# Optimization experiments

Hardware: AMD Instinct MI355X
Metric: run time of the kernel (lower is better)

## Reference

```python
import jax, jax.numpy as jnp
import numpy as np

N = 100_000      # nodes
E = 1_600_000    # edges (avg degree 16)
P = 100_000      # pos/neg sampled edges
L = 3            # GIN layers
D_IN = 128
D_H = 128
D_MLP = 512
D_PRED = D_H // 2
D_FIN = 1


def setup_inputs() -> dict:
    key = jax.random.key(0)
    ks = jax.random.split(key, 12)
    s_in = 1.0 / np.sqrt(D_IN)
    s_mlp = 1.0 / np.sqrt(D_MLP)
    s_h = 1.0 / np.sqrt(D_H)
    s_p = 1.0 / np.sqrt(D_PRED)
    return {
        "x":   jax.random.normal(ks[0], (N, D_IN), jnp.float32),
        "W1":  jax.random.normal(ks[1], (L, D_IN, D_MLP), jnp.float32) * s_in,
        "b1":  jnp.zeros((L, D_MLP), jnp.float32),
        "W2":  jax.random.normal(ks[2], (L, D_MLP, D_H), jnp.float32) * s_mlp,
        "b2":  jnp.zeros((L, D_H), jnp.float32),
        "Wp1": jax.random.normal(ks[3], (D_H, D_PRED), jnp.float32) * s_h,
        "bp1": jnp.zeros((D_PRED,), jnp.float32),
        "Wp2": jax.random.normal(ks[4], (D_PRED, D_FIN), jnp.float32) * s_p,
        "bp2": jnp.zeros((D_FIN,), jnp.float32),
        "edge_src": jax.random.randint(ks[5], (E,), 0, N),
        "edge_dst": jax.random.randint(ks[6], (E,), 0, N),
        "pos_src": jax.random.randint(ks[7], (P,), 0, N),
        "pos_dst": jax.random.randint(ks[8], (P,), 0, N),
        "neg_src": jax.random.randint(ks[9], (P,), 0, N),
        "neg_dst": jax.random.randint(ks[10], (P,), 0, N),
    }


def reference(x, W1, b1, W2, b2, Wp1, bp1, Wp2, bp2,
              edge_src, edge_dst, pos_src, pos_dst, neg_src, neg_dst):
    h = x
    for l in range(L):
        # GINConv 'sum': aggregate neighbor features src->dst, eps=0
        agg = jax.ops.segment_sum(h[edge_src], edge_dst, num_segments=N)
        z = jax.nn.relu((h + agg) @ W1[l] + b1[l])   # [N, D_MLP]
        h = z @ W2[l] + b2[l]                        # [N, D_H]
        h = jax.nn.relu(h)                           # outer ReLU in forward()

    def predict(src, dst):
        z = jax.nn.relu((h[src] * h[dst]) @ Wp1 + bp1)
        return z @ Wp2 + bp2                         # [P, D_FIN]

    h_pos = predict(pos_src, pos_dst)
    h_neg = predict(neg_src, neg_dst)
    return (h_pos, h_neg, h)
```

## Files before the change

kernel.cpp:

```cpp
#include <hip/hip_runtime.h>

typedef unsigned short ushort_t;

constexpr int NN = 100000;
constexpr int EE = 1600000;
constexpr int PP = 100000;
constexpr int DH = 128;
constexpr int DM = 512;

using frag_b16 = __attribute__((ext_vector_type(8))) short;
using frag_f32 = __attribute__((ext_vector_type(4))) float;

union FragU {
  ushort_t s[8];
  uint4 u;
  frag_b16 f;
};

__device__ inline void split_bf16(float x, ushort_t& hi, ushort_t& lo) {
  unsigned int bx = __float_as_uint(x);
  hi = (ushort_t)(bx >> 16);
  float hf = __uint_as_float(bx & 0xFFFF0000u);
  float r = x - hf;
  unsigned int br = __float_as_uint(r);
  unsigned int rb = br + 0x7FFFu + ((br >> 16) & 1u);
  lo = (ushort_t)(rb >> 16);
}

__device__ inline ushort_t rne_bf16(float x) {
  unsigned int u = __float_as_uint(x);
  unsigned int r = u + 0x7FFFu + ((u >> 16) & 1u);
  return (ushort_t)(r >> 16);
}

__device__ inline void bf2x(unsigned int u, float& a, float& b) {
  a = __uint_as_float(u << 16);
  b = __uint_as_float(u & 0xFFFF0000u);
}

__device__ inline void g2l16(const ushort_t* __restrict__ g, ushort_t* l) {
  __builtin_amdgcn_global_load_lds(
      (const __attribute__((address_space(1))) void*)g,
      (__attribute__((address_space(3))) void*)l, 16, 0, 0);
}


__global__ void hist_kernel(const int* __restrict__ dst, int* __restrict__ deg) {
  int i = blockIdx.x * 256 + threadIdx.x;
  if (i < EE) atomicAdd(&deg[dst[i]], 1);
}

__global__ void scan1_kernel(const int* __restrict__ deg, int* __restrict__ inc,
                             int* __restrict__ bsum) {
  __shared__ int buf[2][512];
  int base = blockIdx.x * 512;
  for (int i = threadIdx.x; i < 512; i += 256) {
    int g = base + i;
    buf[0][i] = (g < NN) ? deg[g] : 0;
  }
  __syncthreads();
  int cur = 0;
  for (int off = 1; off < 512; off <<= 1) {
    int nxt = cur ^ 1;
    for (int i = threadIdx.x; i < 512; i += 256) {
      int v = buf[cur][i];
      if (i >= off) v += buf[cur][i - off];
      buf[nxt][i] = v;
    }
    __syncthreads();
    cur = nxt;
  }
  for (int i = threadIdx.x; i < 512; i += 256) {
    int g = base + i;
    if (g < NN) inc[g] = buf[cur][i];
  }
  if (threadIdx.x == 0) bsum[blockIdx.x] = buf[cur][511];
}

__global__ void scan2_kernel(int* __restrict__ bsum, int nb) {
  __shared__ int buf[2][256];
  int i = threadIdx.x;
  buf[0][i] = (i < nb) ? bsum[i] : 0;
  __syncthreads();
  int cur = 0;
  for (int off = 1; off < 256; off <<= 1) {
    int nxt = cur ^ 1;
    int v = buf[cur][i];
    if (i >= off) v += buf[cur][i - off];
    buf[nxt][i] = v;
    __syncthreads();
    cur = nxt;
  }
  if (i < nb) bsum[i] = (i == 0) ? 0 : buf[cur][i - 1];
}

__global__ void scan3_kernel(const int* __restrict__ inc, const int* __restrict__ deg,
                             const int* __restrict__ bsum,
                             int* __restrict__ row_off, int* __restrict__ cursor) {
  int i = blockIdx.x * 256 + threadIdx.x;
  if (i < NN) {
    int excl = inc[i] - deg[i] + bsum[i >> 9];
    row_off[i] = excl;
    cursor[i] = excl;
    if (i == NN - 1) row_off[NN] = excl + deg[i];
  }
}

constexpr int SC_NW = 8;
constexpr int SC_WND = (NN + SC_NW - 1) / SC_NW;
constexpr int SC_EPB = 8192;
constexpr int SC_CHUNKS = (EE + SC_EPB - 1) / SC_EPB;

__global__ __launch_bounds__(256) void scatter_kernel(const int* __restrict__ esrc,
                                                      const int* __restrict__ edst,
                                                      int* __restrict__ cursor,
                                                      int* __restrict__ csr) {
  const int w = blockIdx.x & (SC_NW - 1);
  const int chunk = blockIdx.x / SC_NW;
  const int lo = w * SC_WND;
  const int hi = lo + SC_WND;
  const int base = chunk * SC_EPB;
  #pragma unroll 4
  for (int it = 0; it < SC_EPB / 256; ++it) {
    int i = base + it * 256 + threadIdx.x;
    if (i < EE) {
      int d = edst[i];
      if (d >= lo && d < hi) {
        int p = atomicAdd(&cursor[d], 1);
        csr[p] = esrc[i];
      }
    }
  }
}

__global__ void pack_w1_kernel(const float* __restrict__ W1, ushort_t* __restrict__ wp) {
  int t = blockIdx.x * 256 + threadIdx.x;
  if (t >= 3 * 128 * 64) return;
  int lane = t & 63;
  int tile = t >> 6;
  int tk = tile & 3;
  int tn = (tile >> 2) & 31;
  int layer = tile >> 7;
  int n = tn * 16 + (lane & 15);
  int k0 = tk * 32 + (lane >> 4) * 8;
  const float* src = W1 + (size_t)layer * DH * DM;
  size_t dst = (size_t)t * 8;
  #pragma unroll
  for (int j = 0; j < 8; ++j) wp[dst + j] = rne_bf16(src[(size_t)(k0 + j) * DM + n]);
}

__global__ void pack_w2_kernel(const float* __restrict__ W2, ushort_t* __restrict__ wp) {
  int t = blockIdx.x * 256 + threadIdx.x;
  if (t >= 3 * 128 * 64) return;
  int lane = t & 63;
  int tile = t >> 6;
  int tn = tile & 7;
  int ktg = (tile >> 3) & 15;
  int layer = tile >> 7;
  int n = tn * 16 + (lane & 15);
  int k0 = ktg * 32 + (lane >> 4) * 8;
  const float* src = W2 + (size_t)layer * DM * DH;
  size_t dst = (size_t)t * 8;
  #pragma unroll
  for (int j = 0; j < 8; ++j) wp[dst + j] = rne_bf16(src[(size_t)(k0 + j) * DH + n]);
}

__global__ void cvt_bf16_kernel(const float* __restrict__ x, ushort_t* __restrict__ xb) {
  int i = blockIdx.x * 256 + threadIdx.x;
  if (i < NN * DH / 4) {
    float4 v = ((const float4*)x)[i];
    ushort4 o;
    o.x = rne_bf16(v.x); o.y = rne_bf16(v.y); o.z = rne_bf16(v.z); o.w = rne_bf16(v.w);
    ((ushort4*)xb)[i] = o;
  }
}

__global__ __launch_bounds__(256) void agg_kernel(const ushort_t* __restrict__ hbf,
                                                  const int* __restrict__ row_off,
                                                  const int* __restrict__ csr,
                                                  ushort_t* __restrict__ s_hi,
                                                  ushort_t* __restrict__ s_lo) {
  int t = blockIdx.x * 256 + threadIdx.x;
  int grp = t >> 4;
  int lane = t & 15;
  if (grp >= NN) return;
  const uint4* hp = (const uint4*)hbf;
  float acc[8];
  {
    uint4 v = hp[(size_t)grp * 16 + lane];
    bf2x(v.x, acc[0], acc[1]);
    bf2x(v.y, acc[2], acc[3]);
    bf2x(v.z, acc[4], acc[5]);
    bf2x(v.w, acc[6], acc[7]);
  }
  int e = row_off[grp];
  int e1 = row_off[grp + 1];
  for (; e + 1 < e1; e += 2) {
    uint4 a = hp[(size_t)csr[e] * 16 + lane];
    uint4 b = hp[(size_t)csr[e + 1] * 16 + lane];
    float f0, f1;
    bf2x(a.x, f0, f1); acc[0] += f0; acc[1] += f1;
    bf2x(a.y, f0, f1); acc[2] += f0; acc[3] += f1;
    bf2x(a.z, f0, f1); acc[4] += f0; acc[5] += f1;
    bf2x(a.w, f0, f1); acc[6] += f0; acc[7] += f1;
    bf2x(b.x, f0, f1); acc[0] += f0; acc[1] += f1;
    bf2x(b.y, f0, f1); acc[2] += f0; acc[3] += f1;
    bf2x(b.z, f0, f1); acc[4] += f0; acc[5] += f1;
    bf2x(b.w, f0, f1); acc[6] += f0; acc[7] += f1;
  }
  if (e < e1) {
    uint4 a = hp[(size_t)csr[e] * 16 + lane];
    float f0, f1;
    bf2x(a.x, f0, f1); acc[0] += f0; acc[1] += f1;
    bf2x(a.y, f0, f1); acc[2] += f0; acc[3] += f1;
    bf2x(a.z, f0, f1); acc[4] += f0; acc[5] += f1;
    bf2x(a.w, f0, f1); acc[6] += f0; acc[7] += f1;
  }
  unsigned int hw[4], lw[4];
  #pragma unroll
  for (int i = 0; i < 4; ++i) {
    ushort_t h0, l0, h1, l1;
    split_bf16(acc[2 * i], h0, l0);
    split_bf16(acc[2 * i + 1], h1, l1);
    hw[i] = (unsigned int)h0 | ((unsigned int)h1 << 16);
    lw[i] = (unsigned int)l0 | ((unsigned int)l1 << 16);
  }
  size_t o = (size_t)grp * DH + lane * 8;
  *(uint4*)(s_hi + o) = make_uint4(hw[0], hw[1], hw[2], hw[3]);
  *(uint4*)(s_lo + o) = make_uint4(lw[0], lw[1], lw[2], lw[3]);
}

__global__ __launch_bounds__(256, 2) void mlp_kernel(
    const ushort_t* __restrict__ s_hi, const ushort_t* __restrict__ s_lo,
    const ushort_t* __restrict__ w1p, const float* __restrict__ b1s,
    const ushort_t* __restrict__ w2p, const float* __restrict__ b2s,
    float* __restrict__ hout_f32, ushort_t* __restrict__ hout_bf16) {
  __shared__ ushort_t wA[8 * 512];
  __shared__ ushort_t wB[8 * 512];
  __shared__ float zt[32 * 130];
  const int tid = threadIdx.x;
  const int wave = tid >> 6;
  const int lane = tid & 63;
  const int quad = lane >> 4;
  const int l15 = lane & 15;
  const int m_base = wave * 32;
  const int row0 = blockIdx.x * 128;

  frag_b16 a_hi[2][4], a_lo[2][4];
  #pragma unroll
  for (int ms = 0; ms < 2; ++ms) {
    int gr = row0 + m_base + ms * 16 + l15;
    if (gr >= NN) gr = NN - 1;
    #pragma unroll
    for (int tk = 0; tk < 4; ++tk) {
      size_t o = (size_t)gr * DH + tk * 32 + quad * 8;
      FragU uh, ul;
      uh.u = *(const uint4*)(s_hi + o);
      ul.u = *(const uint4*)(s_lo + o);
      a_hi[ms][tk] = uh.f;
      a_lo[ms][tk] = ul.f;
    }
  }

  frag_f32 hacc[2][8];
  #pragma unroll
  for (int ms = 0; ms < 2; ++ms)
    #pragma unroll
    for (int tn = 0; tn < 8; ++tn) hacc[ms][tn] = {0.f, 0.f, 0.f, 0.f};

  for (int ch = 0; ch < 16; ++ch) {
    #pragma unroll
    for (int i = 0; i < 2; ++i)
      g2l16(w1p + ((size_t)(ch * 512 + i * 256 + tid)) * 8, wA + (i * 256 + tid) * 8);
    #pragma unroll
    for (int i = 0; i < 2; ++i)
      g2l16(w2p + ((size_t)(ch * 512 + i * 256 + tid)) * 8, wB + (i * 256 + tid) * 8);
    __syncthreads();

    frag_f32 za[2][2];
    #pragma unroll
    for (int ms = 0; ms < 2; ++ms)
      #pragma unroll
      for (int tn = 0; tn < 2; ++tn) za[ms][tn] = {0.f, 0.f, 0.f, 0.f};

    #pragma unroll
    for (int tk = 0; tk < 4; ++tk) {
      #pragma unroll
      for (int tn = 0; tn < 2; ++tn) {
        FragU wv;
        wv.u = *(const uint4*)(wA + (tn * 4 + tk) * 512 + lane * 8);
        #pragma unroll
        for (int ms = 0; ms < 2; ++ms) {
          za[ms][tn] = __builtin_amdgcn_mfma_f32_16x16x32_bf16(a_hi[ms][tk], wv.f,
                                                               za[ms][tn], 0, 0, 0);
          za[ms][tn] = __builtin_amdgcn_mfma_f32_16x16x32_bf16(a_lo[ms][tk], wv.f,
                                                               za[ms][tn], 0, 0, 0);
        }
      }
    }

    #pragma unroll
    for (int tn = 0; tn < 2; ++tn) {
      float b1v = b1s[ch * 32 + tn * 16 + l15];
      #pragma unroll
      for (int ms = 0; ms < 2; ++ms) {
        float z0 = fmaxf(za[ms][tn][0] + b1v, 0.f);
        float z1 = fmaxf(za[ms][tn][1] + b1v, 0.f);
        float z2 = fmaxf(za[ms][tn][2] + b1v, 0.f);
        float z3 = fmaxf(za[ms][tn][3] + b1v, 0.f);
        float* zp = &zt[(tn * 16 + l15) * 130 + m_base + ms * 16 + quad * 4];
        *(float2*)zp = make_float2(z0, z1);
        *(float2*)(zp + 2) = make_float2(z2, z3);
      }
    }

    FragU zh[2], zl[2];
    #pragma unroll
    for (int ms = 0; ms < 2; ++ms) {
      #pragma unroll
      for (int j = 0; j < 8; ++j) {
        float v = zt[(quad * 8 + j) * 130 + m_base + ms * 16 + l15];
        split_bf16(v, zh[ms].s[j], zl[ms].s[j]);
      }
    }
    #pragma unroll
    for (int tn = 0; tn < 8; ++tn) {
      FragU wv;
      wv.u = *(const uint4*)(wB + tn * 512 + lane * 8);
      #pragma unroll
      for (int ms = 0; ms < 2; ++ms) {
        hacc[ms][tn] = __builtin_amdgcn_mfma_f32_16x16x32_bf16(zh[ms].f, wv.f,
                                                               hacc[ms][tn], 0, 0, 0);
        hacc[ms][tn] = __builtin_amdgcn_mfma_f32_16x16x32_bf16(zl[ms].f, wv.f,
                                                               hacc[ms][tn], 0, 0, 0);
      }
    }
    __syncthreads();
  }

  #pragma unroll
  for (int tn = 0; tn < 8; ++tn) {
    int col = tn * 16 + l15;
    float b2v = b2s[col];
    #pragma unroll
    for (int ms = 0; ms < 2; ++ms) {
      #pragma unroll
      for (int r = 0; r < 4; ++r) {
        int gr = row0 + m_base + ms * 16 + quad * 4 + r;
        if (gr < NN) {
          float v = fmaxf(hacc[ms][tn][r] + b2v, 0.f);
          if (hout_f32) hout_f32[(size_t)gr * DH + col] = v;
          if (hout_bf16) hout_bf16[(size_t)gr * DH + col] = rne_bf16(v);
        }
      }
    }
  }
}

__global__ __launch_bounds__(256) void predict_kernel(
    const float* __restrict__ h, const int* __restrict__ psrc, const int* __restrict__ pdst,
    const int* __restrict__ nsrc, const int* __restrict__ ndst,
    const float* __restrict__ Wp1, const float* __restrict__ bp1,
    const float* __restrict__ Wp2, const float* __restrict__ bp2,
    float* __restrict__ out) {
  __shared__ float g_tile[64 * 132];
  const int tid = threadIdx.x;
  const int s0 = blockIdx.x * 64;

  #pragma unroll
  for (int i = 0; i < 8; ++i) {
    int idx = tid + i * 256;
    int smp = s0 + (idx >> 5);
    int c4 = (idx & 31) << 2;
    float4 g = make_float4(0.f, 0.f, 0.f, 0.f);
    if (smp < 2 * PP) {
      int si = (smp < PP) ? psrc[smp] : nsrc[smp - PP];
      int di = (smp < PP) ? pdst[smp] : ndst[smp - PP];
      float4 a = *(const float4*)(h + (size_t)si * DH + c4);
      float4 b = *(const float4*)(h + (size_t)di * DH + c4);
      g = make_float4(a.x * b.x, a.y * b.y, a.z * b.z, a.w * b.w);
    }
    *(float4*)(&g_tile[(idx >> 5) * 132 + c4]) = g;
  }
  __syncthreads();

  const int tr = (tid >> 4) << 2;
  const int tc = (tid & 15) << 2;
  float z[4][4];
  #pragma unroll
  for (int r = 0; r < 4; ++r)
    #pragma unroll
    for (int c = 0; c < 4; ++c) z[r][c] = 0.f;

  for (int k = 0; k < DH; ++k) {
    float4 w = *(const float4*)(Wp1 + ((size_t)k << 6) + tc);
    float a[4];
    #pragma unroll
    for (int r = 0; r < 4; ++r) a[r] = g_tile[(tr + r) * 132 + k];
    #pragma unroll
    for (int r = 0; r < 4; ++r) {
      z[r][0] = fmaf(a[r], w.x, z[r][0]);
      z[r][1] = fmaf(a[r], w.y, z[r][1]);
      z[r][2] = fmaf(a[r], w.z, z[r][2]);
      z[r][3] = fmaf(a[r], w.w, z[r][3]);
    }
  }

  float4 b1v = *(const float4*)(bp1 + tc);
  float4 w2v = *(const float4*)(Wp2 + tc);
  float part[4];
  #pragma unroll
  for (int r = 0; r < 4; ++r) {
    part[r] = fmaxf(z[r][0] + b1v.x, 0.f) * w2v.x +
              fmaxf(z[r][1] + b1v.y, 0.f) * w2v.y +
              fmaxf(z[r][2] + b1v.z, 0.f) * w2v.z +
              fmaxf(z[r][3] + b1v.w, 0.f) * w2v.w;
  }
  #pragma unroll
  for (int off = 1; off < 16; off <<= 1) {
    #pragma unroll
    for (int r = 0; r < 4; ++r) part[r] += __shfl_xor(part[r], off, 64);
  }
  if ((tid & 15) == 0) {
    float bias = bp2[0];
    #pragma unroll
    for (int r = 0; r < 4; ++r) {
      int smp = s0 + tr + r;
      if (smp < 2 * PP) out[smp] = part[r] + bias;
    }
  }
}

extern "C" void kernel_launch(void* const* d_in, const int* in_sizes, int n_in,
                              void* d_out, int out_size, void* d_ws, size_t ws_size,
                              hipStream_t stream) {
  const float* x   = (const float*)d_in[0];
  const float* W1  = (const float*)d_in[1];
  const float* b1  = (const float*)d_in[2];
  const float* W2  = (const float*)d_in[3];
  const float* b2  = (const float*)d_in[4];
  const float* Wp1 = (const float*)d_in[5];
  const float* bp1 = (const float*)d_in[6];
  const float* Wp2 = (const float*)d_in[7];
  const float* bp2 = (const float*)d_in[8];
  const int* esrc = (const int*)d_in[9];
  const int* edst = (const int*)d_in[10];
  const int* psrc = (const int*)d_in[11];
  const int* pdst = (const int*)d_in[12];
  const int* nsrc = (const int*)d_in[13];
  const int* ndst = (const int*)d_in[14];

  float* out = (float*)d_out;
  float* out_pred = out;
  float* hbuf = out + 2 * (size_t)PP;
  ushort_t* hbf = (ushort_t*)hbuf;

  char* w = (char*)d_ws;
  ushort_t* s_hi = (ushort_t*)w;
  ushort_t* s_lo = s_hi + (size_t)NN * DH;
  ushort_t* w1p  = s_lo + (size_t)NN * DH;
  ushort_t* w2p  = w1p + 3 * 128 * 64 * 8;
  int* row_off = (int*)(w2p + 3 * 128 * 64 * 8);
  int* csr     = row_off + (NN + 1);
  int* deg    = (int*)w;
  int* inc    = deg + NN;
  int* bsum   = inc + NN;
  int* cursor = bsum + 256;

  hipMemsetAsync(deg, 0, NN * sizeof(int), stream);
  hist_kernel<<<(EE + 255) / 256, 256, 0, stream>>>(edst, deg);
  scan1_kernel<<<(NN + 511) / 512, 256, 0, stream>>>(deg, inc, bsum);
  scan2_kernel<<<1, 256, 0, stream>>>(bsum, (NN + 511) / 512);
  scan3_kernel<<<(NN + 255) / 256, 256, 0, stream>>>(inc, deg, bsum, row_off, cursor);
  scatter_kernel<<<SC_CHUNKS * SC_NW, 256, 0, stream>>>(esrc, edst, cursor, csr);

  pack_w1_kernel<<<96, 256, 0, stream>>>(W1, w1p);
  pack_w2_kernel<<<96, 256, 0, stream>>>(W2, w2p);

  cvt_bf16_kernel<<<(NN * DH / 4 + 255) / 256, 256, 0, stream>>>(x, hbf);

  for (int l = 0; l < 3; ++l) {
    agg_kernel<<<(NN * 16 + 255) / 256, 256, 0, stream>>>(hbf, row_off, csr, s_hi, s_lo);
    mlp_kernel<<<(NN + 127) / 128, 256, 0, stream>>>(
        s_hi, s_lo,
        w1p + (size_t)l * 128 * 64 * 8, b1 + (size_t)l * DM,
        w2p + (size_t)l * 128 * 64 * 8, b2 + (size_t)l * DH,
        (l == 2) ? hbuf : nullptr, (l == 2) ? nullptr : hbf);
  }

  predict_kernel<<<(2 * PP + 63) / 64, 256, 0, stream>>>(
      hbuf, psrc, pdst, nsrc, ndst, Wp1, bp1, Wp2, bp2, out_pred);
}
```

Before: 798.3 us.

## Use bf16 MFMA with hi/lo split for link predictor first layer

Rewrites the predictor's first dense layer to use 16x16x32 bf16 MFMA instead of scalar fp32 FMAs. The gathered edge products are split into hi/lo bf16 pairs and stored in a swizzled LDS tile of 128 samples, and Wp1 is pre-packed into MFMA fragment layout by a new small kernel. This is meant to cut ALU time in the predict kernel. In exchange it uses 64KB of LDS per block, which lowers occupancy for the gather phase, and it introduces bf16 rounding of the weights.

```diff
diff --git a/kernel.cpp b/kernel.cpp
--- a/kernel.cpp
+++ b/kernel.cpp
@@ -165,6 +165,20 @@
   for (int j = 0; j < 8; ++j) wp[dst + j] = rne_bf16(src[(size_t)(k0 + j) * DH + n]);
 }
 
+__global__ void pack_wp1_kernel(const float* __restrict__ Wp1, ushort_t* __restrict__ wp) {
+  int t = blockIdx.x * 256 + threadIdx.x;
+  if (t >= 16 * 64) return;
+  int lane = t & 63;
+  int tile = t >> 6;
+  int tn = tile & 3;
+  int tk = tile >> 2;
+  int n = tn * 16 + (lane & 15);
+  int k0 = tk * 32 + (lane >> 4) * 8;
+  size_t dst = (size_t)t * 8;
+  #pragma unroll
+  for (int j = 0; j < 8; ++j) wp[dst + j] = rne_bf16(Wp1[(size_t)(k0 + j) * 64 + n]);
+}
+
 __global__ void cvt_bf16_kernel(const float* __restrict__ x, ushort_t* __restrict__ xb) {
   int i = blockIdx.x * 256 + threadIdx.x;
   if (i < NN * DH / 4) {
@@ -357,76 +371,109 @@
   }
 }
 
-__global__ __launch_bounds__(256) void predict_kernel(
+__global__ __launch_bounds__(256, 2) void predict_kernel(
     const float* __restrict__ h, const int* __restrict__ psrc, const int* __restrict__ pdst,
     const int* __restrict__ nsrc, const int* __restrict__ ndst,
-    const float* __restrict__ Wp1, const float* __restrict__ bp1,
+    const ushort_t* __restrict__ wp1p, const float* __restrict__ bp1,
     const float* __restrict__ Wp2, const float* __restrict__ bp2,
     float* __restrict__ out) {
-  __shared__ float g_tile[64 * 132];
+  __shared__ unsigned int gp[128 * 128];
   const int tid = threadIdx.x;
-  const int s0 = blockIdx.x * 64;
-
-  #pragma unroll
-  for (int i = 0; i < 8; ++i) {
+  const int wave = tid >> 6;
+  const int lane = tid & 63;
+  const int quad = lane >> 4;
+  const int l15 = lane & 15;
+  const int m_base = wave * 32;
+  const int s0 = blockIdx.x * 128;
+
+  FragU wb1[4][4];
+  #pragma unroll
+  for (int tk = 0; tk < 4; ++tk)
+    #pragma unroll
+    for (int tn = 0; tn < 4; ++tn)
+      wb1[tk][tn].u = *(const uint4*)(wp1p + ((size_t)((tk * 4 + tn) * 64 + lane)) * 8);
+
+  #pragma unroll 8
+  for (int i = 0; i < 16; ++i) {
     int idx = tid + i * 256;
-    int smp = s0 + (idx >> 5);
+    int m = idx >> 5;
     int c4 = (idx & 31) << 2;
-    float4 g = make_float4(0.f, 0.f, 0.f, 0.f);
+    int smp = s0 + m;
+    uint4 pk = make_uint4(0u, 0u, 0u, 0u);
     if (smp < 2 * PP) {
       int si = (smp < PP) ? psrc[smp] : nsrc[smp - PP];
       int di = (smp < PP) ? pdst[smp] : ndst[smp - PP];
       float4 a = *(const float4*)(h + (size_t)si * DH + c4);
       float4 b = *(const float4*)(h + (size_t)di * DH + c4);
-      g = make_float4(a.x * b.x, a.y * b.y, a.z * b.z, a.w * b.w);
-    }
-    *(float4*)(&g_tile[(idx >> 5) * 132 + c4]) = g;
+      ushort_t hh, ll;
+      split_bf16(a.x * b.x, hh, ll); pk.x = (unsigned)hh | ((unsigned)ll << 16);
+      split_bf16(a.y * b.y, hh, ll); pk.y = (unsigned)hh | ((unsigned)ll << 16);
+      split_bf16(a.z * b.z, hh, ll); pk.z = (unsigned)hh | ((unsigned)ll << 16);
+      split_bf16(a.w * b.w, hh, ll); pk.w = (unsigned)hh | ((unsigned)ll << 16);
+    }
+    int slot = (m << 7) + c4;
+    slot ^= (m & 7) << 2;
+    *(uint4*)(gp + slot) = pk;
   }
   __syncthreads();
 
-  const int tr = (tid >> 4) << 2;
-  const int tc = (tid & 15) << 2;
-  float z[4][4];
-  #pragma unroll
-  for (int r = 0; r < 4; ++r)
-    #pragma unroll
-    for (int c = 0; c < 4; ++c) z[r][c] = 0.f;
-
-  for (int k = 0; k < DH; ++k) {
-    float4 w = *(const float4*)(Wp1 + ((size_t)k << 6) + tc);
-    float a[4];
-    #pragma unroll
-    for (int r = 0; r < 4; ++r) a[r] = g_tile[(tr + r) * 132 + k];
+  frag_f32 za[2][4];
+  #pragma unroll
+  for (int ms = 0; ms < 2; ++ms)
+    #pragma unroll
+    for (int tn = 0; tn < 4; ++tn) za[ms][tn] = {0.f, 0.f, 0.f, 0.f};
+
+  #pragma unroll
+  for (int ms = 0; ms < 2; ++ms) {
+    int m = m_base + ms * 16 + l15;
+    int swz = (m & 7) << 2;
+    #pragma unroll
+    for (int tk = 0; tk < 4; ++tk) {
+      int idx0 = (m << 7) + tk * 32 + quad * 8;
+      uint4 u0 = *(const uint4*)(gp + (idx0 ^ swz));
+      uint4 u1 = *(const uint4*)(gp + ((idx0 + 4) ^ swz));
+      unsigned int uu[8];
+      *(uint4*)uu = u0;
+      *(uint4*)(uu + 4) = u1;
+      FragU ah, al;
+      #pragma unroll
+      for (int j = 0; j < 8; ++j) {
+        ah.s[j] = (ushort_t)(uu[j] & 0xFFFFu);
+        al.s[j] = (ushort_t)(uu[j] >> 16);
+      }
+      #pragma unroll
+      for (int tn = 0; tn < 4; ++tn) {
+        za[ms][tn] = __builtin_amdgcn_mfma_f32_16x16x32_bf16(ah.f, wb1[tk][tn].f,
+                                                             za[ms][tn], 0, 0, 0);
+        za[ms][tn] = __builtin_amdgcn_mfma_f32_16x16x32_bf16(al.f, wb1[tk][tn].f,
+                                                             za[ms][tn], 0, 0, 0);
+      }
+    }
+  }
+
+  float b1v[4], w2v[4];
+  #pragma unroll
+  for (int tn = 0; tn < 4; ++tn) {
+    b1v[tn] = bp1[tn * 16 + l15];
+    w2v[tn] = Wp2[tn * 16 + l15];
+  }
+  float bias = bp2[0];
+  #pragma unroll
+  for (int ms = 0; ms < 2; ++ms) {
     #pragma unroll
     for (int r = 0; r < 4; ++r) {
-      z[r][0] = fmaf(a[r], w.x, z[r][0]);
-      z[r][1] = fmaf(a[r], w.y, z[r][1]);
-      z[r][2] = fmaf(a[r], w.z, z[r][2]);
-      z[r][3] = fmaf(a[r], w.w, z[r][3]);
-    }
-  }
-
-  float4 b1v = *(const float4*)(bp1 + tc);
-  float4 w2v = *(const float4*)(Wp2 + tc);
-  float part[4];
-  #pragma unroll
-  for (int r = 0; r < 4; ++r) {
-    part[r] = fmaxf(z[r][0] + b1v.x, 0.f) * w2v.x +
-              fmaxf(z[r][1] + b1v.y, 0.f) * w2v.y +
-              fmaxf(z[r][2] + b1v.z, 0.f) * w2v.z +
-              fmaxf(z[r][3] + b1v.w, 0.f) * w2v.w;
-  }
-  #pragma unroll
-  for (int off = 1; off < 16; off <<= 1) {
-    #pragma unroll
-    for (int r = 0; r < 4; ++r) part[r] += __shfl_xor(part[r], off, 64);
-  }
-  if ((tid & 15) == 0) {
-    float bias = bp2[0];
-    #pragma unroll
-    for (int r = 0; r < 4; ++r) {
-      int smp = s0 + tr + r;
-      if (smp < 2 * PP) out[smp] = part[r] + bias;
+      float p = 0.f;
+      #pragma unroll
+      for (int tn = 0; tn < 4; ++tn)
+        p += fmaxf(za[ms][tn][r] + b1v[tn], 0.f) * w2v[tn];
+      p += __shfl_xor(p, 1, 64);
+      p += __shfl_xor(p, 2, 64);
+      p += __shfl_xor(p, 4, 64);
+      p += __shfl_xor(p, 8, 64);
+      if (l15 == 0) {
+        int smp = s0 + m_base + ms * 16 + quad * 4 + r;
+        if (smp < 2 * PP) out[smp] = p + bias;
+      }
     }
   }
 }
@@ -460,7 +507,8 @@
   ushort_t* s_lo = s_hi + (size_t)NN * DH;
   ushort_t* w1p  = s_lo + (size_t)NN * DH;
   ushort_t* w2p  = w1p + 3 * 128 * 64 * 8;
-  int* row_off = (int*)(w2p + 3 * 128 * 64 * 8);
+  ushort_t* wp1p = w2p + 3 * 128 * 64 * 8;
+  int* row_off = (int*)(wp1p + 16 * 64 * 8);
   int* csr     = row_off + (NN + 1);
   int* deg    = (int*)w;
   int* inc    = deg + NN;
@@ -476,6 +524,7 @@
 
   pack_w1_kernel<<<96, 256, 0, stream>>>(W1, w1p);
   pack_w2_kernel<<<96, 256, 0, stream>>>(W2, w2p);
+  pack_wp1_kernel<<<4, 256, 0, stream>>>(Wp1, wp1p);
 
   cvt_bf16_kernel<<<(NN * DH / 4 + 255) / 256, 256, 0, stream>>>(x, hbf);
 
@@ -488,6 +537,6 @@
         (l == 2) ? hbuf : nullptr, (l == 2) ? nullptr : hbf);
   }
 
-  predict_kernel<<<(2 * PP + 63) / 64, 256, 0, stream>>>(
-      hbuf, psrc, pdst, nsrc, ndst, Wp1, bp1, Wp2, bp2, out_pred);
-}
+  predict_kernel<<<(2 * PP + 127) / 128, 256, 0, stream>>>(
+      hbuf, psrc, pdst, nsrc, ndst, wp1p, bp1, Wp2, bp2, out_pred);
+}
```

Result: faster. 775.3 us (-2.9%).
